# Performance work log

Measured on AMD Instinct MI355X. Metric: run time of the kernel, lower is better.

The kernel has to match this reference:

```python
import jax, jax.numpy as jnp
import numpy as np

G, NPG = 100, 500
N = G * NPG            # 50000 nodes, contiguous equal-size graphs
IN, H = 128, 256
L = 3                  # num_layers
K = 3                  # knn k (loop=True -> self included)
E = 16 * N             # 800000 edges

def setup_inputs():
    key = jax.random.key(0)
    k = jax.random.split(key, 8)
    x = jax.random.normal(k[0], (N, IN), jnp.float32)
    batch = jnp.repeat(jnp.arange(G, dtype=jnp.int32), NPG)
    gid = jax.random.randint(k[1], (E,), 0, G)
    src = jax.random.randint(k[2], (E,), 0, NPG) + gid * NPG
    dst = jax.random.randint(k[3], (E,), 0, NPG) + gid * NPG
    edge_index = jnp.stack([src, dst]).astype(jnp.int32)
    def lin(kk, fin, fout):
        return (jax.random.normal(kk, (fin, fout), jnp.float32) / np.sqrt(fin)).astype(jnp.float32)
    inp = dict(x=x, edge_index=edge_index, batch=batch)
    inp["emb_W"] = lin(k[4], IN, H); inp["emb_b"] = jnp.zeros((H,), jnp.float32)
    inp["conv_W"] = jnp.stack([lin(jax.random.fold_in(k[5], i), H, H) for i in range(L)])
    inp["conv_b"] = jnp.zeros((L, H), jnp.float32)
    inp["fconv_W"] = jnp.stack([lin(jax.random.fold_in(k[6], i), H, H) for i in range(L)])
    inp["fconv_b"] = jnp.zeros((L, H), jnp.float32)
    inp["norm_w"] = jnp.ones((L, H), jnp.float32); inp["norm_b"] = jnp.zeros((L, H), jnp.float32); inp["norm_ms"] = jnp.ones((L, H), jnp.float32)
    inp["fnorm_w"] = jnp.ones((L, H), jnp.float32); inp["fnorm_b"] = jnp.zeros((L, H), jnp.float32); inp["fnorm_ms"] = jnp.ones((L, H), jnp.float32)
    inp["gate_W"] = lin(k[7], 2 * H, H); inp["gate_b"] = jnp.zeros((H,), jnp.float32)
    return inp

def _gcn_conv(h, src, dst, W, b):
    # GCNConv: add self loops, symmetric deg^-1/2 normalization
    m = h @ W                                     # [N,H]
    loop = jnp.arange(N, dtype=src.dtype)
    s2 = jnp.concatenate([src, loop]); d2 = jnp.concatenate([dst, loop])
    deg = jax.ops.segment_sum(jnp.ones_like(d2, jnp.float32), d2, num_segments=N)
    dinv = jnp.where(deg > 0, jax.lax.rsqrt(deg), 0.0)
    coef = (dinv[s2] * dinv[d2])[:, None]
    return jax.ops.segment_sum(m[s2] * coef, d2, num_segments=N) + b

def _graph_norm(x, batch, w, b, ms, cnt):
    # PyG GraphNorm: out = w * (x - ms*mean) / sqrt(var + eps) + b, per-graph stats
    mean = jax.ops.segment_sum(x, batch, num_segments=G) / cnt
    out = x - mean[batch] * ms
    var = jax.ops.segment_sum(out * out, batch, num_segments=G) / cnt
    return w * out * jax.lax.rsqrt(var + 1e-5)[batch] + b

def _knn_graph(x):
    # per-graph cosine knn, loop=True (self has sim 1 and is kept)
    xr = x.reshape(G, NPG, -1)
    xn = xr / (jnp.linalg.norm(xr, axis=-1, keepdims=True) + 1e-12)
    sim = jnp.einsum('gnh,gmh->gnm', xn, xn)      # [G,NPG,NPG]
    _, idx = jax.lax.top_k(sim, K)                # [G,NPG,K]
    offs = (jnp.arange(G) * NPG)[:, None, None]
    src = (idx + offs).reshape(-1)
    dst = jnp.broadcast_to(jnp.arange(N).reshape(G, NPG, 1), (G, NPG, K)).reshape(-1)
    return src.astype(jnp.int32), dst.astype(jnp.int32)

def reference(x, edge_index, batch, emb_W, emb_b, conv_W, conv_b, norm_w, norm_b, norm_ms, fconv_W, fconv_b, fnorm_w, fnorm_b, fnorm_ms, gate_W, gate_b):
    cnt = jax.ops.segment_sum(jnp.ones((N,), jnp.float32), batch, num_segments=G)[:, None]
    h = x @ emb_W + emb_b
    fsrc, fdst = _knn_graph(h)
    src, dst = edge_index[0], edge_index[1]
    all_x = []
    for i in range(L - 1):   # eval mode: dropout is identity
        prev = h
        h = _gcn_conv(h, src, dst, conv_W[i], conv_b[i])
        h = jax.nn.leaky_relu(_graph_norm(h, batch, norm_w[i], norm_b[i], norm_ms[i], cnt))
        f = _gcn_conv(h, fsrc, fdst, fconv_W[i], fconv_b[i])
        f = jax.nn.leaky_relu(_graph_norm(f, batch, fnorm_w[i], fnorm_b[i], fnorm_ms[i], cnt))
        gate = jax.nn.sigmoid(jnp.concatenate([h, f], axis=-1) @ gate_W + gate_b)
        h = gate * h + (1.0 - gate) * f + prev
        all_x.append(h)
    # faithful to source: for i in range(L): += pool(all_x[i-1])  (Python negative indexing!)
    gf = jnp.zeros((G, H), jnp.float32)
    for i in range(L):
        gf = gf + jax.ops.segment_sum(all_x[i - 1], batch, num_segments=G) / cnt
    return gf
```

## Files before the change

kernel.cpp:

```cpp
#include <hip/hip_runtime.h>
#include <math.h>

#define NN 50000
#define GG 100
#define NPGc 500
#define HH 256
#define IND 128

typedef __attribute__((ext_vector_type(8))) short short8v;
typedef __attribute__((ext_vector_type(4))) float f32x4;

__device__ __forceinline__ ushort f2bf(float f) {
    union { float f; unsigned u; } v; v.f = f;
    unsigned r = (v.u + 0x7fffu + ((v.u >> 16) & 1u)) >> 16;
    return (ushort)r;
}
__device__ __forceinline__ float bf2f(ushort h) {
    union { unsigned u; float f; } v; v.u = ((unsigned)h) << 16;
    return v.f;
}

__device__ __forceinline__ int swz(int row, int kidx) { return kidx ^ ((row & 7) << 3); }

__global__ void wcvt(const float* __restrict__ src, ushort* __restrict__ dst, int K, int N)
{
    int i = blockIdx.x * 256 + threadIdx.x;
    if (i < K * N) {
        int n = i / K, k = i % K;
        dst[i] = f2bf(src[(size_t)k * N + n]);
    }
}

__global__ __launch_bounds__(256)
void gemm_mfma(const float* __restrict__ A, const float* __restrict__ A2,
               const ushort* __restrict__ Wt, const float* __restrict__ bias,
               float* __restrict__ C, int M, int K, int lda, int mode,
               const float* __restrict__ hn, const float* __restrict__ fn,
               const float* __restrict__ prev)
{
    __shared__ ushort As[128][64];
    __shared__ ushort Bs[128][64];
    const int tid = threadIdx.x;
    const int lane = tid & 63;
    const int w = tid >> 6;
    const int wr = (w >> 1) * 64, wc = (w & 1) * 64;
    const int row0 = blockIdx.x * 128, col0 = blockIdx.y * 128;
    const int lr = lane & 15, lk = (lane >> 4) * 8;
    f32x4 acc[4][4] = {};

    for (int k0 = 0; k0 < K; k0 += 64) {
        __syncthreads();
        #pragma unroll
        for (int it = 0; it < 4; ++it) {
            int c = it * 256 + tid;
            int row = c >> 3, col = (c & 7) * 8;
            int gr = row0 + row; if (gr > M - 1) gr = M - 1;
            const float* Ap = A; int kk = k0 + col;
            if (A2 != nullptr && kk >= 256) { Ap = A2; kk -= 256; }
            const float* s = &Ap[(size_t)gr * lda + kk];
            float4 v0 = *(const float4*)s;
            float4 v1 = *(const float4*)(s + 4);
            union { ushort u[8]; int4 q; } pk;
            pk.u[0] = f2bf(v0.x); pk.u[1] = f2bf(v0.y); pk.u[2] = f2bf(v0.z); pk.u[3] = f2bf(v0.w);
            pk.u[4] = f2bf(v1.x); pk.u[5] = f2bf(v1.y); pk.u[6] = f2bf(v1.z); pk.u[7] = f2bf(v1.w);
            *(int4*)&As[row][swz(row, col)] = pk.q;
        }
        #pragma unroll
        for (int it = 0; it < 4; ++it) {
            int c = it * 256 + tid;
            int n = c >> 3, k = (c & 7) * 8;
            *(int4*)&Bs[n][swz(n, k)] = *(const int4*)&Wt[(size_t)(col0 + n) * K + k0 + k];
        }
        __syncthreads();
        #pragma unroll
        for (int ks = 0; ks < 2; ++ks) {
            short8v av[4], bv[4];
            #pragma unroll
            for (int m = 0; m < 4; ++m) {
                int rr = wr + m * 16 + lr;
                av[m] = *(const short8v*)&As[rr][swz(rr, ks * 32 + lk)];
            }
            #pragma unroll
            for (int n = 0; n < 4; ++n) {
                int rr = wc + n * 16 + lr;
                bv[n] = *(const short8v*)&Bs[rr][swz(rr, ks * 32 + lk)];
            }
            #pragma unroll
            for (int m = 0; m < 4; ++m)
                #pragma unroll
                for (int n = 0; n < 4; ++n)
                    acc[m][n] = __builtin_amdgcn_mfma_f32_16x16x32_bf16(av[m], bv[n], acc[m][n], 0, 0, 0);
        }
    }
    const int fr = (lane >> 4) * 4;
    if (mode == 0) {
        #pragma unroll
        for (int n = 0; n < 4; ++n) {
            int col = col0 + wc + n * 16 + lr;
            float bb = bias ? bias[col] : 0.f;
            #pragma unroll
            for (int m = 0; m < 4; ++m) {
                int rbase = row0 + wr + m * 16 + fr;
                #pragma unroll
                for (int r = 0; r < 4; ++r) {
                    int row = rbase + r;
                    if (row < M) C[(size_t)row * HH + col] = acc[m][n][r] + bb;
                }
            }
        }
    } else {
        #pragma unroll
        for (int n = 0; n < 4; ++n) {
            int col = col0 + wc + n * 16 + lr;
            float gb = bias[col];
            #pragma unroll
            for (int m = 0; m < 4; ++m) {
                int rbase = row0 + wr + m * 16 + fr;
                #pragma unroll
                for (int r = 0; r < 4; ++r) {
                    int row = rbase + r;
                    if (row < M) {
                        size_t o = (size_t)row * HH + col;
                        float z = acc[m][n][r] + gb;
                        float s = 1.f / (1.f + expf(-z));
                        C[o] = s * hn[o] + (1.f - s) * fn[o] + prev[o];
                    }
                }
            }
        }
    }
}

__global__ __launch_bounds__(256)
void row_norm_hl(const float* __restrict__ h, ushort* __restrict__ xh, ushort* __restrict__ xl)
{
    int n = blockIdx.x, c = threadIdx.x;
    float v = h[(size_t)n * HH + c];
    __shared__ float red[256];
    red[c] = v * v;
    __syncthreads();
    for (int s = 128; s > 0; s >>= 1) {
        if (c < s) red[c] += red[c + s];
        __syncthreads();
    }
    float norm = sqrtf(red[0]);
    float xn = v / (norm + 1e-12f);
    ushort hi = f2bf(xn);
    xh[(size_t)n * HH + c] = hi;
    xl[(size_t)n * HH + c] = f2bf(xn - bf2f(hi));
}

__device__ __forceinline__ bool tk_better(float va, int ia, float vb, int ib)
{
    return (va > vb) || (va == vb && ia < ib);
}

__device__ __forceinline__ void ins3(float v, int i,
                                     float& a0, int& b0, float& a1, int& b1,
                                     float& a2, int& b2)
{
    if (tk_better(v, i, a0, b0))      { a2 = a1; b2 = b1; a1 = a0; b1 = b0; a0 = v; b0 = i; }
    else if (tk_better(v, i, a1, b1)) { a2 = a1; b2 = b1; a1 = v;  b1 = i; }
    else if (tk_better(v, i, a2, b2)) { a2 = v;  b2 = i; }
}

__device__ __forceinline__ void merge3(float& v0, float& v1, float& v2,
                                       int& i0, int& i1, int& i2, int off)
{
    float w0 = __shfl_xor(v0, off), w1 = __shfl_xor(v1, off), w2 = __shfl_xor(v2, off);
    int   j0 = __shfl_xor(i0, off), j1 = __shfl_xor(i1, off), j2 = __shfl_xor(i2, off);
    float avv[3] = { v0, v1, v2 }, bvv[3] = { w0, w1, w2 };
    int   aii[3] = { i0, i1, i2 }, bii[3] = { j0, j1, j2 };
    float rv[3]; int ri[3];
    int p = 0, q = 0;
    #pragma unroll
    for (int t = 0; t < 3; ++t) {
        bool takeA = tk_better(avv[p], aii[p], bvv[q], bii[q]);
        rv[t] = takeA ? avv[p] : bvv[q];
        ri[t] = takeA ? aii[p] : bii[q];
        if (takeA) ++p; else ++q;
    }
    v0 = rv[0]; v1 = rv[1]; v2 = rv[2];
    i0 = ri[0]; i1 = ri[1]; i2 = ri[2];
}

__global__ __launch_bounds__(256, 2)
void simtopk(const ushort* __restrict__ xnh, const ushort* __restrict__ xnl,
             int* __restrict__ fsrc)
{
    __shared__ ushort Bs[2][2][128][36];
    const int bid = blockIdx.x;
    const int xcd = bid & 7;
    const int rb  = (bid >> 3) & 7;
    const int g   = (bid >> 6) * 8 + xcd;
    if (g >= GG) return;
    const int row0 = rb * 64;
    const int tid  = threadIdx.x;
    const int lane = tid & 63;
    const int w    = tid >> 6;
    const int lr   = lane & 15;
    const int hi4  = lane >> 4;
    const size_t base = (size_t)g * NPGc * HH;

    int arow = row0 + w * 16 + lr; if (arow > NPGc - 1) arow = NPGc - 1;
    const ushort* aph = xnh + base + (size_t)arow * HH + hi4 * 8;
    const ushort* apl = xnl + base + (size_t)arow * HH + hi4 * 8;
    short8v ah[8], al[8];
    #pragma unroll
    for (int kc = 0; kc < 8; ++kc) {
        ah[kc] = *(const short8v*)(aph + kc * 32);
        al[kc] = *(const short8v*)(apl + kc * 32);
    }

    const int scol = tid >> 1;
    const int sq   = (tid & 1) * 2;

    float tv0[4], tv1[4], tv2[4];
    int   ti0[4], ti1[4], ti2[4];
    #pragma unroll
    for (int r = 0; r < 4; ++r) {
        tv0[r] = tv1[r] = tv2[r] = -2.f;
        ti0[r] = ti1[r] = ti2[r] = 0x7fffffff;
    }

    for (int ct = 0; ct < 4; ++ct) {
        const int col0 = ct * 128;
        int gcol = col0 + scol; if (gcol > NPGc - 1) gcol = NPGc - 1;
        const ushort* sph = xnh + base + (size_t)gcol * HH + sq * 8;
        const ushort* spl = xnl + base + (size_t)gcol * HH + sq * 8;

        {
            int4 h0 = *(const int4*)(sph);
            int4 h1 = *(const int4*)(sph + 8);
            int4 l0 = *(const int4*)(spl);
            int4 l1 = *(const int4*)(spl + 8);
            *(int4*)&Bs[0][0][scol][sq * 8]     = h0;
            *(int4*)&Bs[0][0][scol][sq * 8 + 8] = h1;
            *(int4*)&Bs[0][1][scol][sq * 8]     = l0;
            *(int4*)&Bs[0][1][scol][sq * 8 + 8] = l1;
        }
        __syncthreads();

        f32x4 acc[8] = {};
        #pragma unroll
        for (int kc = 0; kc < 8; ++kc) {
            const int cur = kc & 1, nxt = cur ^ 1;
            int4 h0, h1, l0, l1;
            if (kc < 7) {
                const ushort* nh = sph + (kc + 1) * 32;
                const ushort* nl = spl + (kc + 1) * 32;
                h0 = *(const int4*)(nh);
                h1 = *(const int4*)(nh + 8);
                l0 = *(const int4*)(nl);
                l1 = *(const int4*)(nl + 8);
            }
            short8v bh[8], bl[8];
            #pragma unroll
            for (int n = 0; n < 8; ++n) {
                int rr = n * 16 + lr;
                bh[n] = *(const short8v*)&Bs[cur][0][rr][hi4 * 8];
                bl[n] = *(const short8v*)&Bs[cur][1][rr][hi4 * 8];
            }
            #pragma unroll
            for (int n = 0; n < 8; ++n) {
                acc[n] = __builtin_amdgcn_mfma_f32_16x16x32_bf16(ah[kc], bh[n], acc[n], 0, 0, 0);
                acc[n] = __builtin_amdgcn_mfma_f32_16x16x32_bf16(ah[kc], bl[n], acc[n], 0, 0, 0);
                acc[n] = __builtin_amdgcn_mfma_f32_16x16x32_bf16(al[kc], bh[n], acc[n], 0, 0, 0);
            }
            if (kc < 7) {
                *(int4*)&Bs[nxt][0][scol][sq * 8]     = h0;
                *(int4*)&Bs[nxt][0][scol][sq * 8 + 8] = h1;
                *(int4*)&Bs[nxt][1][scol][sq * 8]     = l0;
                *(int4*)&Bs[nxt][1][scol][sq * 8 + 8] = l1;
            }
            __syncthreads();
        }

        #pragma unroll
        for (int n = 0; n < 8; ++n) {
            int col = col0 + n * 16 + lr;
            if (col < NPGc) {
                #pragma unroll
                for (int r = 0; r < 4; ++r)
                    ins3(acc[n][r], col, tv0[r], ti0[r], tv1[r], ti1[r], tv2[r], ti2[r]);
            }
        }
    }

    #pragma unroll
    for (int r = 0; r < 4; ++r) {
        #pragma unroll
        for (int off = 1; off <= 8; off <<= 1)
            merge3(tv0[r], tv1[r], tv2[r], ti0[r], ti1[r], ti2[r], off);
    }

    if (lr == 0) {
        #pragma unroll
        for (int r = 0; r < 4; ++r) {
            int row = row0 + w * 16 + hi4 * 4 + r;
            if (row < NPGc) {
                int rg = g * NPGc + row;
                fsrc[rg * 3 + 0] = g * NPGc + ti0[r];
                fsrc[rg * 3 + 1] = g * NPGc + ti1[r];
                fsrc[rg * 3 + 2] = g * NPGc + ti2[r];
            }
        }
    }
}

__global__ void hist_kernel(const int* __restrict__ dst, int* __restrict__ cnt, int nE)
{
    int e = blockIdx.x * 256 + threadIdx.x;
    if (e < nE) atomicAdd(&cnt[dst[e]], 1);
}

__global__ void scan1_kernel(const int* __restrict__ in, int* __restrict__ out,
                             int* __restrict__ bsum, int n)
{
    __shared__ int sh[256];
    int t = threadIdx.x;
    int i = blockIdx.x * 256 + t;
    int v = (i < n) ? in[i] : 0;
    sh[t] = v;
    __syncthreads();
    for (int s = 1; s < 256; s <<= 1) {
        int tv = (t >= s) ? sh[t - s] : 0;
        __syncthreads();
        sh[t] += tv;
        __syncthreads();
    }
    if (i < n) out[i] = sh[t] - v;
    if (t == 255) bsum[blockIdx.x] = sh[255];
}

__global__ void scan2_kernel(int* __restrict__ bsum, int nb)
{
    __shared__ int sh[256];
    int t = threadIdx.x;
    int v = (t < nb) ? bsum[t] : 0;
    sh[t] = v;
    __syncthreads();
    for (int s = 1; s < 256; s <<= 1) {
        int tv = (t >= s) ? sh[t - s] : 0;
        __syncthreads();
        sh[t] += tv;
        __syncthreads();
    }
    if (t < nb) bsum[t] = sh[t] - v;
}

__global__ void scan3_kernel(int* __restrict__ out, const int* __restrict__ bsum, int n)
{
    int i = blockIdx.x * 256 + threadIdx.x;
    if (i < n) out[i] += bsum[blockIdx.x];
}

__global__ void fill_kernel(const int* __restrict__ src, const int* __restrict__ dst,
                            const int* __restrict__ row_ptr, int* __restrict__ cursor,
                            int* __restrict__ sorted_src, int nE)
{
    int e = blockIdx.x * 256 + threadIdx.x;
    if (e < nE) {
        int d = dst[e];
        int pos = row_ptr[d] + atomicAdd(&cursor[d], 1);
        sorted_src[pos] = src[e];
    }
}

__global__ void dinv_kernel(const int* __restrict__ cnt, float* __restrict__ dinv, int n)
{
    int i = blockIdx.x * 256 + threadIdx.x;
    if (i < n) dinv[i] = rsqrtf((float)cnt[i] + 1.0f);
}

__global__ __launch_bounds__(256)
void gcn_gather(const float* __restrict__ m, const int* __restrict__ row_ptr,
                const int* __restrict__ cnt, const int* __restrict__ srcs,
                const float* __restrict__ dinv, const float* __restrict__ bias,
                float* __restrict__ out)
{
    int n = blockIdx.x, c = threadIdx.x;
    float dn = dinv[n];
    float acc = m[(size_t)n * HH + c] * dn;
    int s0 = row_ptr[n], e0 = s0 + cnt[n];
    for (int e = s0; e < e0; ++e) {
        int s = srcs[e];
        acc += m[(size_t)s * HH + c] * dinv[s];
    }
    out[(size_t)n * HH + c] = acc * dn + bias[c];
}

__global__ __launch_bounds__(256)
void fgcn_gather(const float* __restrict__ m, const int* __restrict__ fsrc,
                 const float* __restrict__ bias, float* __restrict__ out)
{
    int n = blockIdx.x, c = threadIdx.x;
    int s0 = fsrc[n * 3], s1 = fsrc[n * 3 + 1], s2 = fsrc[n * 3 + 2];
    float acc = m[(size_t)n * HH + c] + m[(size_t)s0 * HH + c]
              + m[(size_t)s1 * HH + c] + m[(size_t)s2 * HH + c];
    out[(size_t)n * HH + c] = 0.25f * acc + bias[c];
}

__global__ __launch_bounds__(256)
void norm_stats(const float* __restrict__ x, float* __restrict__ S1, float* __restrict__ S2)
{
    int g = blockIdx.x, chunk = blockIdx.y, c = threadIdx.x;
    int r0 = chunk * 63, r1 = min(r0 + 63, NPGc);
    float s1 = 0.f, s2 = 0.f;
    for (int r = r0; r < r1; ++r) {
        float v = x[((size_t)(g * NPGc + r)) * HH + c];
        s1 += v; s2 += v * v;
    }
    atomicAdd(&S1[g * HH + c], s1);
    atomicAdd(&S2[g * HH + c], s2);
}

__global__ __launch_bounds__(256)
void norm_apply(float* __restrict__ x, const float* __restrict__ S1, const float* __restrict__ S2,
                const float* __restrict__ w, const float* __restrict__ b,
                const float* __restrict__ ms)
{
    int n = blockIdx.x, c = threadIdx.x;
    int g = n / NPGc;
    size_t o = (size_t)n * HH + c;
    float v = x[o];
    float mean = S1[g * HH + c] / (float)NPGc;
    float mm = mean * ms[c];
    float var = S2[g * HH + c] / (float)NPGc - 2.f * mm * mean + mm * mm;
    float outv = w[c] * (v - mm) * rsqrtf(var + 1e-5f) + b[c];
    x[o] = outv > 0.f ? outv : 0.01f * outv;
}

__global__ __launch_bounds__(256)
void pool_kernel(const float* __restrict__ X0, const float* __restrict__ X1,
                 float* __restrict__ out)
{
    int g = blockIdx.x, c = threadIdx.x;
    float s0 = 0.f, s1 = 0.f;
    for (int r = 0; r < NPGc; ++r) {
        size_t o = ((size_t)(g * NPGc + r)) * HH + c;
        s0 += X0[o];
        s1 += X1[o];
    }
    out[g * HH + c] = (s0 + 2.f * s1) / (float)NPGc;
}

__global__ void sentinel_kernel(float* out, int n)
{
    int i = blockIdx.x * 256 + threadIdx.x;
    if (i < n) out[i] = 12345.0f;
}

extern "C" void kernel_launch(void* const* d_in, const int* in_sizes, int n_in,
                              void* d_out, int out_size, void* d_ws, size_t ws_size,
                              hipStream_t stream)
{
    const float* x       = (const float*)d_in[0];
    const int* edge_idx  = (const int*)d_in[1];
    const float* emb_W   = (const float*)d_in[3];
    const float* emb_b   = (const float*)d_in[4];
    const float* conv_W  = (const float*)d_in[5];
    const float* conv_b  = (const float*)d_in[6];
    const float* fconv_W = (const float*)d_in[7];
    const float* fconv_b = (const float*)d_in[8];
    const float* norm_w  = (const float*)d_in[9];
    const float* norm_b  = (const float*)d_in[10];
    const float* norm_ms = (const float*)d_in[11];
    const float* fnorm_w = (const float*)d_in[12];
    const float* fnorm_b = (const float*)d_in[13];
    const float* fnorm_ms= (const float*)d_in[14];
    const float* gate_W  = (const float*)d_in[15];
    const float* gate_b  = (const float*)d_in[16];

    const int E = in_sizes[1] / 2;
    const int* esrc = edge_idx;
    const int* edst = edge_idx + E;

    const size_t NHf = (size_t)NN * HH;
    char* p = (char*)d_ws;
    auto alloc = [&](size_t bytes) { char* r = p; p += (bytes + 255) & ~(size_t)255; return r; };
    float* B0 = (float*)alloc(NHf * 4);
    float* B1 = (float*)alloc(NHf * 4);
    float* B2 = (float*)alloc(NHf * 4);
    float* B3 = (float*)alloc(NHf * 4);
    ushort* xnh = (ushort*)B2;
    ushort* xnl = xnh + NHf;
    int* sorted_src = (int*)alloc((size_t)E * 4);
    int* row_ptr    = (int*)alloc((size_t)NN * 4);
    int* deg_cnt    = (int*)alloc((size_t)NN * 4);
    int* cursor     = (int*)alloc((size_t)NN * 4);
    float* dinv     = (float*)alloc((size_t)NN * 4);
    int* fsrc       = (int*)alloc((size_t)NN * 3 * 4);
    float* S1       = (float*)alloc((size_t)GG * HH * 4);
    float* S2       = (float*)alloc((size_t)GG * HH * 4);
    int* bsum       = (int*)alloc(1024);
    ushort* wts     = (ushort*)alloc((size_t)425984 * 2);
    size_t needed = (size_t)(p - (char*)d_ws);
    if (ws_size < needed) {
        sentinel_kernel<<<(out_size + 255) / 256, 256, 0, stream>>>((float*)d_out, out_size);
        return;
    }
    ushort* embWt   = wts;
    ushort* convWt0 = wts + 32768;
    ushort* convWt1 = wts + 32768 + 65536;
    ushort* fconvWt0 = wts + 163840;
    ushort* fconvWt1 = wts + 163840 + 65536;
    ushort* gateWt  = wts + 294912;

    const int nScanB = (NN + 255) / 256;

    hipMemsetAsync(deg_cnt, 0, (size_t)NN * 4, stream);
    hipMemsetAsync(cursor, 0, (size_t)NN * 4, stream);

    wcvt<<<(32768 + 255) / 256, 256, 0, stream>>>(emb_W, embWt, IND, HH);
    wcvt<<<(65536 + 255) / 256, 256, 0, stream>>>(conv_W, convWt0, HH, HH);
    wcvt<<<(65536 + 255) / 256, 256, 0, stream>>>(conv_W + 65536, convWt1, HH, HH);
    wcvt<<<(65536 + 255) / 256, 256, 0, stream>>>(fconv_W, fconvWt0, HH, HH);
    wcvt<<<(65536 + 255) / 256, 256, 0, stream>>>(fconv_W + 65536, fconvWt1, HH, HH);
    wcvt<<<(131072 + 255) / 256, 256, 0, stream>>>(gate_W, gateWt, 2 * HH, HH);

    dim3 ggrid((NN + 127) / 128, 2);
    gemm_mfma<<<ggrid, 256, 0, stream>>>(x, nullptr, embWt, emb_b, B0, NN, IND, IND, 0,
                                         nullptr, nullptr, nullptr);

    hist_kernel<<<(E + 255) / 256, 256, 0, stream>>>(edst, deg_cnt, E);
    scan1_kernel<<<nScanB, 256, 0, stream>>>(deg_cnt, row_ptr, bsum, NN);
    scan2_kernel<<<1, 256, 0, stream>>>(bsum, nScanB);
    scan3_kernel<<<nScanB, 256, 0, stream>>>(row_ptr, bsum, NN);
    fill_kernel<<<(E + 255) / 256, 256, 0, stream>>>(esrc, edst, row_ptr, cursor, sorted_src, E);
    dinv_kernel<<<(NN + 255) / 256, 256, 0, stream>>>(deg_cnt, dinv, NN);

    row_norm_hl<<<NN, 256, 0, stream>>>(B0, xnh, xnl);
    simtopk<<<832, 256, 0, stream>>>(xnh, xnl, fsrc);

    float* h  = B0;
    float* mb = B1;
    dim3 ngrid(GG, 8);
    for (int i = 0; i < 2; ++i) {
        const ushort* Wc = (i == 0) ? convWt0 : convWt1;
        const ushort* Wf = (i == 0) ? fconvWt0 : fconvWt1;
        const float* bc  = conv_b  + (size_t)i * HH;
        const float* bf  = fconv_b + (size_t)i * HH;
        gemm_mfma<<<ggrid, 256, 0, stream>>>(h, nullptr, Wc, nullptr, mb, NN, HH, HH, 0,
                                             nullptr, nullptr, nullptr);
        gcn_gather<<<NN, 256, 0, stream>>>(mb, row_ptr, deg_cnt, sorted_src, dinv, bc, B2);
        hipMemsetAsync(S1, 0, (size_t)2 * GG * HH * 4, stream);
        norm_stats<<<ngrid, 256, 0, stream>>>(B2, S1, S2);
        norm_apply<<<NN, 256, 0, stream>>>(B2, S1, S2, norm_w + i * HH, norm_b + i * HH,
                                           norm_ms + i * HH);
        gemm_mfma<<<ggrid, 256, 0, stream>>>(B2, nullptr, Wf, nullptr, mb, NN, HH, HH, 0,
                                             nullptr, nullptr, nullptr);
        fgcn_gather<<<NN, 256, 0, stream>>>(mb, fsrc, bf, B3);
        hipMemsetAsync(S1, 0, (size_t)2 * GG * HH * 4, stream);
        norm_stats<<<ngrid, 256, 0, stream>>>(B3, S1, S2);
        norm_apply<<<NN, 256, 0, stream>>>(B3, S1, S2, fnorm_w + i * HH, fnorm_b + i * HH,
                                           fnorm_ms + i * HH);
        gemm_mfma<<<ggrid, 256, 0, stream>>>(B2, B3, gateWt, gate_b, mb, NN, 2 * HH, HH, 1,
                                             B2, B3, h);
        float* t = h; h = mb; mb = t;
    }
    pool_kernel<<<GG, 256, 0, stream>>>(mb, h, (float*)d_out);
}
```

Measured before the change: 1.371 ms.

## Store GCN messages in bf16 and group gather blocks per graph on XCDs

The conv and fconv GEMMs now write their message matrices as bf16 through a new epilogue mode. The gather kernels read and accumulate these bf16 messages, which halves the bytes of the random-access gathers. Gather blocks are remapped so each graph's nodes land on one XCD, improving L2 locality for intra-graph neighbour reads. It also lowers simtopk's occupancy hint from 2 to 1, and it adds bf16 rounding error to the aggregated features.

After: 1.296 ms. 5.5% less time.

```diff
diff --git a/kernel.cpp b/kernel.cpp
--- a/kernel.cpp
+++ b/kernel.cpp
@@ -34,7 +34,8 @@
 __global__ __launch_bounds__(256)
 void gemm_mfma(const float* __restrict__ A, const float* __restrict__ A2,
                const ushort* __restrict__ Wt, const float* __restrict__ bias,
-               float* __restrict__ C, int M, int K, int lda, int mode,
+               float* __restrict__ C, ushort* __restrict__ Cbf,
+               int M, int K, int lda, int mode,
                const float* __restrict__ hn, const float* __restrict__ fn,
                const float* __restrict__ prev)
 {
@@ -108,6 +109,21 @@
                 }
             }
         }
+    } else if (mode == 2) {
+        #pragma unroll
+        for (int n = 0; n < 4; ++n) {
+            int col = col0 + wc + n * 16 + lr;
+            float bb = bias ? bias[col] : 0.f;
+            #pragma unroll
+            for (int m = 0; m < 4; ++m) {
+                int rbase = row0 + wr + m * 16 + fr;
+                #pragma unroll
+                for (int r = 0; r < 4; ++r) {
+                    int row = rbase + r;
+                    if (row < M) Cbf[(size_t)row * HH + col] = f2bf(acc[m][n][r] + bb);
+                }
+            }
+        }
     } else {
         #pragma unroll
         for (int n = 0; n < 4; ++n) {
@@ -184,7 +200,7 @@
     i0 = ri[0]; i1 = ri[1]; i2 = ri[2];
 }
 
-__global__ __launch_bounds__(256, 2)
+__global__ __launch_bounds__(256, 1)
 void simtopk(const ushort* __restrict__ xnh, const ushort* __restrict__ xnl,
              int* __restrict__ fsrc)
 {
@@ -374,30 +390,40 @@
 }
 
 __global__ __launch_bounds__(256)
-void gcn_gather(const float* __restrict__ m, const int* __restrict__ row_ptr,
+void gcn_gather(const ushort* __restrict__ m, const int* __restrict__ row_ptr,
                 const int* __restrict__ cnt, const int* __restrict__ srcs,
                 const float* __restrict__ dinv, const float* __restrict__ bias,
                 float* __restrict__ out)
 {
-    int n = blockIdx.x, c = threadIdx.x;
+    int bid = blockIdx.x;
+    int xcd = bid & 7, idx = bid >> 3;
+    int g = xcd + 8 * (idx / NPGc);
+    if (g >= GG) return;
+    int n = g * NPGc + (idx % NPGc);
+    int c = threadIdx.x;
     float dn = dinv[n];
-    float acc = m[(size_t)n * HH + c] * dn;
+    float acc = bf2f(m[(size_t)n * HH + c]) * dn;
     int s0 = row_ptr[n], e0 = s0 + cnt[n];
     for (int e = s0; e < e0; ++e) {
         int s = srcs[e];
-        acc += m[(size_t)s * HH + c] * dinv[s];
+        acc += bf2f(m[(size_t)s * HH + c]) * dinv[s];
     }
     out[(size_t)n * HH + c] = acc * dn + bias[c];
 }
 
 __global__ __launch_bounds__(256)
-void fgcn_gather(const float* __restrict__ m, const int* __restrict__ fsrc,
+void fgcn_gather(const ushort* __restrict__ m, const int* __restrict__ fsrc,
                  const float* __restrict__ bias, float* __restrict__ out)
 {
-    int n = blockIdx.x, c = threadIdx.x;
+    int bid = blockIdx.x;
+    int xcd = bid & 7, idx = bid >> 3;
+    int g = xcd + 8 * (idx / NPGc);
+    if (g >= GG) return;
+    int n = g * NPGc + (idx % NPGc);
+    int c = threadIdx.x;
     int s0 = fsrc[n * 3], s1 = fsrc[n * 3 + 1], s2 = fsrc[n * 3 + 2];
-    float acc = m[(size_t)n * HH + c] + m[(size_t)s0 * HH + c]
-              + m[(size_t)s1 * HH + c] + m[(size_t)s2 * HH + c];
+    float acc = bf2f(m[(size_t)n * HH + c]) + bf2f(m[(size_t)s0 * HH + c])
+              + bf2f(m[(size_t)s1 * HH + c]) + bf2f(m[(size_t)s2 * HH + c]);
     out[(size_t)n * HH + c] = 0.25f * acc + bias[c];
 }
 
@@ -485,6 +511,7 @@
     float* B3 = (float*)alloc(NHf * 4);
     ushort* xnh = (ushort*)B2;
     ushort* xnl = xnh + NHf;
+    ushort* msgbf = (ushort*)alloc(NHf * 2);
     int* sorted_src = (int*)alloc((size_t)E * 4);
     int* row_ptr    = (int*)alloc((size_t)NN * 4);
     int* deg_cnt    = (int*)alloc((size_t)NN * 4);
@@ -508,6 +535,7 @@
     ushort* gateWt  = wts + 294912;
 
     const int nScanB = (NN + 255) / 256;
+    const int gatherGrid = 8 * 13 * NPGc;
 
     hipMemsetAsync(deg_cnt, 0, (size_t)NN * 4, stream);
     hipMemsetAsync(cursor, 0, (size_t)NN * 4, stream);
@@ -520,8 +548,8 @@
     wcvt<<<(131072 + 255) / 256, 256, 0, stream>>>(gate_W, gateWt, 2 * HH, HH);
 
     dim3 ggrid((NN + 127) / 128, 2);
-    gemm_mfma<<<ggrid, 256, 0, stream>>>(x, nullptr, embWt, emb_b, B0, NN, IND, IND, 0,
-                                         nullptr, nullptr, nullptr);
+    gemm_mfma<<<ggrid, 256, 0, stream>>>(x, nullptr, embWt, emb_b, B0, nullptr,
+                                         NN, IND, IND, 0, nullptr, nullptr, nullptr);
 
     hist_kernel<<<(E + 255) / 256, 256, 0, stream>>>(edst, deg_cnt, E);
     scan1_kernel<<<nScanB, 256, 0, stream>>>(deg_cnt, row_ptr, bsum, NN);
@@ -541,22 +569,23 @@
         const ushort* Wf = (i == 0) ? fconvWt0 : fconvWt1;
         const float* bc  = conv_b  + (size_t)i * HH;
         const float* bf  = fconv_b + (size_t)i * HH;
-        gemm_mfma<<<ggrid, 256, 0, stream>>>(h, nullptr, Wc, nullptr, mb, NN, HH, HH, 0,
-                                             nullptr, nullptr, nullptr);
-        gcn_gather<<<NN, 256, 0, stream>>>(mb, row_ptr, deg_cnt, sorted_src, dinv, bc, B2);
+        gemm_mfma<<<ggrid, 256, 0, stream>>>(h, nullptr, Wc, nullptr, nullptr, msgbf,
+                                             NN, HH, HH, 2, nullptr, nullptr, nullptr);
+        gcn_gather<<<gatherGrid, 256, 0, stream>>>(msgbf, row_ptr, deg_cnt, sorted_src,
+                                                   dinv, bc, B2);
         hipMemsetAsync(S1, 0, (size_t)2 * GG * HH * 4, stream);
         norm_stats<<<ngrid, 256, 0, stream>>>(B2, S1, S2);
         norm_apply<<<NN, 256, 0, stream>>>(B2, S1, S2, norm_w + i * HH, norm_b + i * HH,
                                            norm_ms + i * HH);
-        gemm_mfma<<<ggrid, 256, 0, stream>>>(B2, nullptr, Wf, nullptr, mb, NN, HH, HH, 0,
-                                             nullptr, nullptr, nullptr);
-        fgcn_gather<<<NN, 256, 0, stream>>>(mb, fsrc, bf, B3);
+        gemm_mfma<<<ggrid, 256, 0, stream>>>(B2, nullptr, Wf, nullptr, nullptr, msgbf,
+                                             NN, HH, HH, 2, nullptr, nullptr, nullptr);
+        fgcn_gather<<<gatherGrid, 256, 0, stream>>>(msgbf, fsrc, bf, B3);
         hipMemsetAsync(S1, 0, (size_t)2 * GG * HH * 4, stream);
         norm_stats<<<ngrid, 256, 0, stream>>>(B3, S1, S2);
         norm_apply<<<NN, 256, 0, stream>>>(B3, S1, S2, fnorm_w + i * HH, fnorm_b + i * HH,
                                            fnorm_ms + i * HH);
-        gemm_mfma<<<ggrid, 256, 0, stream>>>(B2, B3, gateWt, gate_b, mb, NN, 2 * HH, HH, 1,
-                                             B2, B3, h);
+        gemm_mfma<<<ggrid, 256, 0, stream>>>(B2, B3, gateWt, gate_b, mb, nullptr,
+                                             NN, 2 * HH, HH, 1, B2, B3, h);
         float* t = h; h = mb; mb = t;
     }
     pool_kernel<<<GG, 256, 0, stream>>>(mb, h, (float*)d_out);
```
